# Optimization experiments

Measured on AMD Instinct MI355X. Metric: run time of the kernel, lower is better.

The kernel has to match this reference:

```python
import jax, jax.numpy as jnp
import numpy as np

NUM_EXPERTS = 8
D_MODEL = 768
D_FF = 4 * D_MODEL


def setup_inputs() -> dict:
    key = jax.random.key(0)
    ks = jax.random.split(key, 7)
    s = 0.02
    x = jax.random.normal(ks[0], (2, 1024, D_MODEL), dtype=jnp.float32)
    router_w = jax.random.normal(ks[1], (D_MODEL, NUM_EXPERTS), dtype=jnp.float32) * s
    router_b = jnp.zeros((NUM_EXPERTS,), dtype=jnp.float32)
    w1 = jax.random.normal(ks[2], (NUM_EXPERTS, D_MODEL, D_FF), dtype=jnp.float32) * s
    b1 = jnp.zeros((NUM_EXPERTS, D_FF), dtype=jnp.float32)
    w2 = jax.random.normal(ks[3], (NUM_EXPERTS, D_FF, D_MODEL), dtype=jnp.float32) * s
    b2 = jnp.zeros((NUM_EXPERTS, D_MODEL), dtype=jnp.float32)
    return {"x": x, "router_w": router_w, "router_b": router_b,
            "w1": w1, "b1": b1, "w2": w2, "b2": b2}


def reference(x, router_w, router_b, w1, b1, w2, b2):
    B, S, D = x.shape
    x_flat = x.reshape(-1, D)                      # [T, D]
    logits = x_flat @ router_w + router_b          # [T, E]
    probs = jax.nn.softmax(logits, axis=-1)
    expert_idx = jnp.argmax(probs, axis=-1)        # [T] int, top-1 routing
    onehot = jax.nn.one_hot(expert_idx, NUM_EXPERTS, dtype=x.dtype)  # [T, E]

    # Per-expert FFN; combine via top-1 one-hot (output is NOT scaled by prob,
    # matching the original). Dropout is eval-mode identity.
    out = jnp.zeros_like(x_flat)
    for e in range(NUM_EXPERTS):
        h = jax.nn.relu(x_flat @ w1[e] + b1[e])    # [T, D_FF]
        y = h @ w2[e] + b2[e]                      # [T, D]
        out = out + onehot[:, e:e + 1] * y
    outputs = out.reshape(B, S, D)

    # Load-balance loss: MSE between empirical expert usage and uniform.
    usage = jnp.bincount(expert_idx, length=NUM_EXPERTS).astype(jnp.float32)
    usage = usage / usage.sum()
    uniform = jnp.full((NUM_EXPERTS,), 1.0 / NUM_EXPERTS, dtype=jnp.float32)
    load_balance_loss = jnp.mean((usage - uniform) ** 2)
    return outputs, load_balance_loss
```

## Files before the change

### kernel.cpp

```cpp
#include <hip/hip_runtime.h>
#include <hip/hip_bf16.h>

#define NTOK 2048
#define DMODEL 768
#define DFF 3072
#define NEXP 8
#define MAXT 24

typedef short bf16x8 __attribute__((ext_vector_type(8)));
typedef float f32x4 __attribute__((ext_vector_type(4)));

typedef __attribute__((address_space(1))) const char GCHAR;
typedef __attribute__((address_space(3))) char LCHAR;
#define GL16(g, l) __builtin_amdgcn_global_load_lds((GCHAR*)(g), (LCHAR*)(l), 16, 0, 0)

template <int K, int N>
__device__ void transpose_tile(const float* __restrict__ W, __hip_bfloat16* __restrict__ WT,
                               int e, int k0, int n0, float* T) {
  const int t = threadIdx.x;
  {
    const int kr = t >> 4;
    const int nc = (t & 15) * 4;
    const float* src = W + ((size_t)e * K + k0) * N + n0;
#pragma unroll
    for (int i = 0; i < 4; i++) {
      float4 v = *(const float4*)(src + (size_t)(kr + i * 16) * N + nc);
      T[(kr + i * 16) * 65 + nc + 0] = v.x;
      T[(kr + i * 16) * 65 + nc + 1] = v.y;
      T[(kr + i * 16) * 65 + nc + 2] = v.z;
      T[(kr + i * 16) * 65 + nc + 3] = v.w;
    }
  }
  __syncthreads();
  {
    const int n = t >> 2;
    const int kq = (t & 3) * 16;
    __align__(16) __hip_bfloat16 u[16];
#pragma unroll
    for (int j = 0; j < 16; j++) u[j] = __float2bfloat16(T[(kq + j) * 65 + n]);
    __hip_bfloat16* dst = WT + ((size_t)e * N + n0 + n) * K + k0 + kq;
    *(int4*)dst = *(const int4*)&u[0];
    *(int4*)(dst + 8) = *(const int4*)&u[8];
  }
}

__global__ __launch_bounds__(256) void k_router_t1(
    const float* __restrict__ x, const float* __restrict__ rw,
    const float* __restrict__ rb, __hip_bfloat16* __restrict__ xbf,
    int* __restrict__ eidx, int* __restrict__ cnt,
    const float* __restrict__ w1, __hip_bfloat16* __restrict__ wT1) {
  __shared__ float T[64 * 65];
  if (blockIdx.x >= 512) {
    int tb = blockIdx.x - 512;
    int n_i = tb % (DFF / 64);
    int k_i = (tb / (DFF / 64)) % (DMODEL / 64);
    int e = tb / ((DFF / 64) * (DMODEL / 64));
    transpose_tile<DMODEL, DFF>(w1, wT1, e, k_i * 64, n_i * 64, T);
    return;
  }
  int tok = (blockIdx.x * blockDim.x + threadIdx.x) >> 6;
  int lane = threadIdx.x & 63;
  if (tok >= NTOK) return;
  const float* xr = x + (size_t)tok * DMODEL;
  double acc[NEXP];
#pragma unroll
  for (int e = 0; e < NEXP; e++) acc[e] = 0.0;
  for (int d0 = 0; d0 < DMODEL; d0 += 64) {
    float v = xr[d0 + lane];
    xbf[(size_t)tok * DMODEL + d0 + lane] = __float2bfloat16(v);
    const float* wrow = rw + (size_t)(d0 + lane) * NEXP;
#pragma unroll
    for (int e = 0; e < NEXP; e++) acc[e] += (double)v * (double)wrow[e];
  }
#pragma unroll
  for (int e = 0; e < NEXP; e++) {
    double a = acc[e];
#pragma unroll
    for (int s = 32; s > 0; s >>= 1) a += __shfl_xor(a, s);
    acc[e] = a;
  }
  if (lane == 0) {
    int best = 0;
    double bv = acc[0] + (double)rb[0];
#pragma unroll
    for (int e = 1; e < NEXP; e++) {
      double v = acc[e] + (double)rb[e];
      if (v > bv) { bv = v; best = e; }
    }
    eidx[tok] = best;
    atomicAdd(&cnt[best], 1);
  }
}

__global__ void k_scan(const int* __restrict__ cnt, int* __restrict__ off,
                       int* __restrict__ cur, float* __restrict__ loss,
                       int* __restrict__ tiles, int* __restrict__ ntile) {
  if (threadIdx.x == 0) {
    int s = 0;
    float l = 0.f;
    int nt = 0;
    for (int e = 0; e < NEXP; e++) {
      off[e] = s;
      cur[e] = s;
      for (int m = 0; m < cnt[e]; m += 128) tiles[nt++] = (e << 20) | m;
      s += cnt[e];
      float u = (float)cnt[e] / (float)NTOK - 1.0f / (float)NEXP;
      l += u * u;
    }
    *ntile = nt;
    *loss = l / (float)NEXP;
  }
}

__global__ __launch_bounds__(256) void k_build(const int* __restrict__ eidx,
                                               int* __restrict__ cur,
                                               int* __restrict__ list) {
  int t = blockIdx.x * blockDim.x + threadIdx.x;
  if (t < NTOK) {
    int e = eidx[t];
    int p = atomicAdd(&cur[e], 1);
    list[p] = t;
  }
}

template <int K_TOT, int KCHUNK, int N, int NSPLIT, bool RELU_BF16, bool GATHER_A,
          bool ATOMIC_C, int TK, int TN>
__global__ __launch_bounds__(256) void k_gemm5(
    const __hip_bfloat16* __restrict__ A, const __hip_bfloat16* __restrict__ BT,
    const float* __restrict__ bias, void* __restrict__ Cout,
    const int* __restrict__ cnt, const int* __restrict__ off,
    const int* __restrict__ list, const int* __restrict__ tiles,
    const int* __restrict__ ntile, const float* __restrict__ Tsrc,
    __hip_bfloat16* __restrict__ Tdst) {
  constexpr int NX = N / 128;
  constexpr int W = NX * MAXT * NSPLIT;
  __shared__ __align__(16) char smem[49152];

  if constexpr (TK > 0) {
    if (blockIdx.x >= W) {
      int tb = blockIdx.x - W;
      int n_i = tb % (TN / 64);
      int k_i = (tb / (TN / 64)) % (TK / 64);
      int e = tb / ((TN / 64) * (TK / 64));
      transpose_tile<TK, TN>(Tsrc, Tdst, e, k_i * 64, n_i * 64, (float*)smem);
      return;
    }
  }

  int b = blockIdx.x;
  constexpr int q = W / 8, r = W % 8;
  const int xcd = b & 7, ii = b >> 3;
  const int widx = (xcd < r ? xcd * (q + 1) : r * (q + 1) + (xcd - r) * q) + ii;
  const int split = widx % NSPLIT;
  const int rest = widx / NSPLIT;
  const int ti = rest % MAXT;
  const int nx = rest / MAXT;
  if (ti >= *ntile) return;
  const int tv = tiles[ti];
  const int e = tv >> 20;
  const int m0 = tv & 0xFFFFF;
  const int ce = cnt[e];
  const int oe = off[e];
  const int n0 = nx * 128;
  const int kbase = split * KCHUNK;

  const int tid = threadIdx.x;
  const int lane = tid & 63;
  const int w = tid >> 6;
  const int wr = (w >> 1) * 64;
  const int wc = (w & 1) * 64;
  const int fr = lane & 15;
  const int hi = lane >> 4;

  const int srow = tid >> 2;
  const int cch = (tid & 3) ^ ((tid >> 3) & 3);

  const __hip_bfloat16* ga[2];
#pragma unroll
  for (int j = 0; j < 2; j++) {
    int mr = m0 + j * 64 + srow;
    int src;
    if (GATHER_A) {
      src = list[oe + (mr < ce ? mr : 0)];
    } else {
      int p2 = oe + mr;
      src = p2 < NTOK ? p2 : NTOK - 1;
    }
    ga[j] = A + (size_t)src * K_TOT + kbase + cch * 8;
  }
  const __hip_bfloat16* gb[2];
#pragma unroll
  for (int j = 0; j < 2; j++) {
    int nr = n0 + j * 64 + srow;
    gb[j] = BT + ((size_t)e * N + nr) * K_TOT + kbase + cch * 8;
  }

  char* lA = smem + tid * 16;

  f32x4 acc[4][4] = {};
  constexpr int NT = KCHUNK / 32;

#define STAGE(buf, kc)                                \
  do {                                                \
    GL16(ga[0] + (kc), lA + (buf)*16384 + 0);         \
    GL16(ga[1] + (kc), lA + (buf)*16384 + 4096);      \
    GL16(gb[0] + (kc), lA + (buf)*16384 + 8192);      \
    GL16(gb[1] + (kc), lA + (buf)*16384 + 12288);     \
  } while (0)

  STAGE(0, 0);
  STAGE(1, 32);
  int cur = 0, sb = 2;
  const int xr = (fr >> 1) & 3;
#pragma unroll 1
  for (int t = 0; t < NT; ++t) {
    if (t + 2 < NT) {
      STAGE(sb, (t + 2) * 32);
      asm volatile("s_waitcnt vmcnt(8)" ::: "memory");
    } else if (t + 1 < NT) {
      asm volatile("s_waitcnt vmcnt(4)" ::: "memory");
    } else {
      asm volatile("s_waitcnt vmcnt(0)" ::: "memory");
    }
    __builtin_amdgcn_s_barrier();
    {
      const char* bA = smem + cur * 16384;
      const char* bB = bA + 8192;
      bf16x8 fa[4], fb[4];
#pragma unroll
      for (int mf = 0; mf < 4; mf++) {
        const int row = wr + mf * 16 + fr;
        fa[mf] = *(const bf16x8*)(bA + row * 64 + ((hi ^ xr) * 16));
      }
#pragma unroll
      for (int nf = 0; nf < 4; nf++) {
        const int row = wc + nf * 16 + fr;
        fb[nf] = *(const bf16x8*)(bB + row * 64 + ((hi ^ xr) * 16));
      }
#pragma unroll
      for (int mf = 0; mf < 4; mf++)
#pragma unroll
        for (int nf = 0; nf < 4; nf++)
          acc[mf][nf] = __builtin_amdgcn_mfma_f32_16x16x32_bf16(fa[mf], fb[nf],
                                                                acc[mf][nf], 0, 0, 0);
    }
    __builtin_amdgcn_s_barrier();
    cur = (cur == 2) ? 0 : cur + 1;
    sb = (sb == 2) ? 0 : sb + 1;
  }
#undef STAGE

#pragma unroll
  for (int mf = 0; mf < 4; mf++) {
#pragma unroll
    for (int jj = 0; jj < 4; jj++) {
      const int mloc = m0 + wr + mf * 16 + hi * 4 + jj;
      if (mloc >= ce) continue;
      if (RELU_BF16) {
        __hip_bfloat16* C = (__hip_bfloat16*)Cout;
        size_t row = (size_t)(oe + mloc) * N;
        const float* bi = bias + (size_t)e * N;
#pragma unroll
        for (int nf = 0; nf < 4; nf++) {
          int nn = n0 + wc + nf * 16 + fr;
          float v = acc[mf][nf][jj] + bi[nn];
          C[row + nn] = __float2bfloat16(v > 0.f ? v : 0.f);
        }
      } else {
        float* C = (float*)Cout;
        int tok = list[oe + mloc];
        size_t row = (size_t)tok * N;
        const float* bi = bias + (size_t)e * N;
#pragma unroll
        for (int nf = 0; nf < 4; nf++) {
          int nn = n0 + wc + nf * 16 + fr;
          float v = acc[mf][nf][jj] + (split == 0 ? bi[nn] : 0.f);
          if (ATOMIC_C)
            atomicAdd(&C[row + nn], v);
          else
            C[row + nn] = v;
        }
      }
    }
  }
}

template <int K, int N, bool RELU_BF16, bool GATHER_A, bool SCATTER_C>
__global__ __launch_bounds__(256) void k_gemm(
    const __hip_bfloat16* __restrict__ A, const float* __restrict__ Bw,
    const float* __restrict__ bias, void* __restrict__ Cout,
    const int* __restrict__ cnt, const int* __restrict__ off,
    const int* __restrict__ list) {
  const int e = blockIdx.z;
  const int ce = cnt[e];
  const int m0 = blockIdx.y * 128;
  if (m0 >= ce) return;
  const int oe = off[e];
  const int n0 = blockIdx.x * 128;

  __shared__ __hip_bfloat16 Asm[128][32];
  __shared__ __hip_bfloat16 Bsm[128][32];

  const int tid = threadIdx.x;
  const int ra = tid >> 1;
  const int ha = (tid & 1) * 16;
  size_t arow;
  {
    int mr = m0 + ra;
    int src;
    if (GATHER_A) {
      src = (mr < ce) ? list[oe + mr] : list[oe];
    } else {
      int p = oe + mr;
      src = (p < NTOK) ? p : (NTOK - 1);
    }
    arow = (size_t)src * K;
  }
  const int rbk = tid >> 3;
  const int nb = (tid & 7) * 16;
  const float* bsrc0 = Bw + ((size_t)e * K + rbk) * N + n0 + nb;

  const int w = tid >> 6;
  const int lane = tid & 63;
  const int wr = (w >> 1) * 64;
  const int wc = (w & 1) * 64;
  const int fr = lane & 15;
  const int fk = (lane >> 4) * 8;

  f32x4 acc[4][4] = {};

  for (int k0 = 0; k0 < K; k0 += 32) {
    __syncthreads();
    {
      const __hip_bfloat16* s = A + arow + k0 + ha;
      int4 v0 = *(const int4*)(s);
      int4 v1 = *(const int4*)(s + 8);
      *(int4*)(&Asm[ra][ha]) = v0;
      *(int4*)(&Asm[ra][ha + 8]) = v1;
    }
    {
      const float* s = bsrc0 + (size_t)k0 * N;
      float4 f0 = *(const float4*)(s);
      float4 f1 = *(const float4*)(s + 4);
      float4 f2 = *(const float4*)(s + 8);
      float4 f3 = *(const float4*)(s + 12);
      __hip_bfloat16* dst = &Bsm[nb][0] + rbk;
      dst[0 * 32] = __float2bfloat16(f0.x);
      dst[1 * 32] = __float2bfloat16(f0.y);
      dst[2 * 32] = __float2bfloat16(f0.z);
      dst[3 * 32] = __float2bfloat16(f0.w);
      dst[4 * 32] = __float2bfloat16(f1.x);
      dst[5 * 32] = __float2bfloat16(f1.y);
      dst[6 * 32] = __float2bfloat16(f1.z);
      dst[7 * 32] = __float2bfloat16(f1.w);
      dst[8 * 32] = __float2bfloat16(f2.x);
      dst[9 * 32] = __float2bfloat16(f2.y);
      dst[10 * 32] = __float2bfloat16(f2.z);
      dst[11 * 32] = __float2bfloat16(f2.w);
      dst[12 * 32] = __float2bfloat16(f3.x);
      dst[13 * 32] = __float2bfloat16(f3.y);
      dst[14 * 32] = __float2bfloat16(f3.z);
      dst[15 * 32] = __float2bfloat16(f3.w);
    }
    __syncthreads();

    bf16x8 fa[4], fb[4];
#pragma unroll
    for (int mf = 0; mf < 4; mf++) fa[mf] = *(const bf16x8*)(&Asm[wr + mf * 16 + fr][fk]);
#pragma unroll
    for (int nf = 0; nf < 4; nf++) fb[nf] = *(const bf16x8*)(&Bsm[wc + nf * 16 + fr][fk]);
#pragma unroll
    for (int mf = 0; mf < 4; mf++)
#pragma unroll
      for (int nf = 0; nf < 4; nf++)
        acc[mf][nf] = __builtin_amdgcn_mfma_f32_16x16x32_bf16(fa[mf], fb[nf], acc[mf][nf], 0, 0, 0);
  }

#pragma unroll
  for (int mf = 0; mf < 4; mf++) {
#pragma unroll
    for (int j = 0; j < 4; j++) {
      const int mloc = m0 + wr + mf * 16 + (lane >> 4) * 4 + j;
      if (mloc >= ce) continue;
      if (RELU_BF16) {
        __hip_bfloat16* C = (__hip_bfloat16*)Cout;
        size_t row = (size_t)(oe + mloc) * N;
        const float* bi = bias + (size_t)e * N;
#pragma unroll
        for (int nf = 0; nf < 4; nf++) {
          int nn = n0 + wc + nf * 16 + fr;
          float v = acc[mf][nf][j] + bi[nn];
          C[row + nn] = __float2bfloat16(v > 0.f ? v : 0.f);
        }
      } else {
        float* C = (float*)Cout;
        int tok = SCATTER_C ? list[oe + mloc] : (oe + mloc);
        size_t row = (size_t)tok * N;
        const float* bi = bias + (size_t)e * N;
#pragma unroll
        for (int nf = 0; nf < 4; nf++) {
          int nn = n0 + wc + nf * 16 + fr;
          C[row + nn] = acc[mf][nf][j] + bi[nn];
        }
      }
    }
  }
}

extern "C" void kernel_launch(void* const* d_in, const int* in_sizes, int n_in,
                              void* d_out, int out_size, void* d_ws, size_t ws_size,
                              hipStream_t stream) {
  const float* x = (const float*)d_in[0];
  const float* rw = (const float*)d_in[1];
  const float* rb = (const float*)d_in[2];
  const float* w1 = (const float*)d_in[3];
  const float* b1 = (const float*)d_in[4];
  const float* w2 = (const float*)d_in[5];
  const float* b2 = (const float*)d_in[6];
  float* out = (float*)d_out;

  char* ws = (char*)d_ws;
  int* cnt = (int*)(ws + 0);
  int* off = (int*)(ws + 32);
  int* cur = (int*)(ws + 64);
  int* ntile = (int*)(ws + 96);
  int* tiles = (int*)(ws + 128);
  int* eidx = (int*)(ws + 512);
  int* list = (int*)(ws + 8704);
  __hip_bfloat16* xbf = (__hip_bfloat16*)(ws + 65536);
  __hip_bfloat16* h = (__hip_bfloat16*)(ws + 4194304);
  __hip_bfloat16* wT1 = (__hip_bfloat16*)(ws + 20971520);
  __hip_bfloat16* wT2 = (__hip_bfloat16*)(ws + 58720256);

  float* loss = out + (size_t)2 * 1024 * 768;
  const size_t REQ = 58720256ull + 37748736ull;

  (void)hipMemsetAsync(cnt, 0, 96, stream);
  (void)hipMemsetAsync(d_out, 0, (size_t)out_size * sizeof(float), stream);

  if (ws_size >= REQ) {
    const int TBLK = (DMODEL / 64) * (DFF / 64) * NEXP;
    k_router_t1<<<512 + TBLK, 256, 0, stream>>>(x, rw, rb, xbf, eidx, cnt, w1, wT1);
    k_scan<<<1, 64, 0, stream>>>(cnt, off, cur, loss, tiles, ntile);
    k_build<<<8, 256, 0, stream>>>(eidx, cur, list);
    k_gemm5<DMODEL, DMODEL, DFF, 1, true, true, false, DFF, DMODEL>
        <<<(DFF / 128) * MAXT + TBLK, 256, 0, stream>>>(
            xbf, wT1, b1, h, cnt, off, list, tiles, ntile, w2, wT2);
    k_gemm5<DFF, DFF / 4, DMODEL, 4, false, false, true, 0, 64>
        <<<(DMODEL / 128) * MAXT * 4, 256, 0, stream>>>(
            h, wT2, b2, out, cnt, off, list, tiles, ntile, nullptr, nullptr);
  } else {
    k_router_t1<<<512, 256, 0, stream>>>(x, rw, rb, xbf, eidx, cnt, w1, wT1);
    k_scan<<<1, 64, 0, stream>>>(cnt, off, cur, loss, tiles, ntile);
    k_build<<<8, 256, 0, stream>>>(eidx, cur, list);
    k_gemm<DMODEL, DFF, true, true, false>
        <<<dim3(DFF / 128, 16, NEXP), 256, 0, stream>>>(xbf, w1, b1, h, cnt, off, list);
    k_gemm<DFF, DMODEL, false, false, true>
        <<<dim3(DMODEL / 128, 16, NEXP), 256, 0, stream>>>(h, w2, b2, out, cnt, off, list);
  }
}
```

Before: 152.4 us.

## Fuse fp32 weight conversion into GEMM loads and replace atomics with partial-sum reduce

Drops the separate transpose-to-bf16 passes over w1 and w2. The GEMM now loads fp32 weights directly into registers, converts them to bf16 and writes them swizzled into LDS, using a register-prefetched pipeline four steps deep. The second GEMM writes per-split partial sums to a workspace instead of doing atomicAdd into the output, and a new reduce kernel sums the four splits and adds the bias, which also removes the output memset. The intent is to avoid writing and re-reading bf16 weight copies every call, at the cost of reading fp32 weights and extra partial-buffer traffic and register pressure.

```diff
diff --git a/kernel.cpp b/kernel.cpp
--- a/kernel.cpp
+++ b/kernel.cpp
@@ -14,50 +14,15 @@
 typedef __attribute__((address_space(3))) char LCHAR;
 #define GL16(g, l) __builtin_amdgcn_global_load_lds((GCHAR*)(g), (LCHAR*)(l), 16, 0, 0)
 
-template <int K, int N>
-__device__ void transpose_tile(const float* __restrict__ W, __hip_bfloat16* __restrict__ WT,
-                               int e, int k0, int n0, float* T) {
-  const int t = threadIdx.x;
-  {
-    const int kr = t >> 4;
-    const int nc = (t & 15) * 4;
-    const float* src = W + ((size_t)e * K + k0) * N + n0;
-#pragma unroll
-    for (int i = 0; i < 4; i++) {
-      float4 v = *(const float4*)(src + (size_t)(kr + i * 16) * N + nc);
-      T[(kr + i * 16) * 65 + nc + 0] = v.x;
-      T[(kr + i * 16) * 65 + nc + 1] = v.y;
-      T[(kr + i * 16) * 65 + nc + 2] = v.z;
-      T[(kr + i * 16) * 65 + nc + 3] = v.w;
-    }
-  }
-  __syncthreads();
-  {
-    const int n = t >> 2;
-    const int kq = (t & 3) * 16;
-    __align__(16) __hip_bfloat16 u[16];
-#pragma unroll
-    for (int j = 0; j < 16; j++) u[j] = __float2bfloat16(T[(kq + j) * 65 + n]);
-    __hip_bfloat16* dst = WT + ((size_t)e * N + n0 + n) * K + k0 + kq;
-    *(int4*)dst = *(const int4*)&u[0];
-    *(int4*)(dst + 8) = *(const int4*)&u[8];
-  }
-}
-
-__global__ __launch_bounds__(256) void k_router_t1(
+__device__ __forceinline__ unsigned int bfu(float v) {
+  __hip_bfloat16 b = __float2bfloat16(v);
+  return (unsigned int)*(unsigned short*)&b;
+}
+
+__global__ __launch_bounds__(256) void k_router(
     const float* __restrict__ x, const float* __restrict__ rw,
     const float* __restrict__ rb, __hip_bfloat16* __restrict__ xbf,
-    int* __restrict__ eidx, int* __restrict__ cnt,
-    const float* __restrict__ w1, __hip_bfloat16* __restrict__ wT1) {
-  __shared__ float T[64 * 65];
-  if (blockIdx.x >= 512) {
-    int tb = blockIdx.x - 512;
-    int n_i = tb % (DFF / 64);
-    int k_i = (tb / (DFF / 64)) % (DMODEL / 64);
-    int e = tb / ((DFF / 64) * (DMODEL / 64));
-    transpose_tile<DMODEL, DFF>(w1, wT1, e, k_i * 64, n_i * 64, T);
-    return;
-  }
+    int* __restrict__ eidx, int* __restrict__ cnt) {
   int tok = (blockIdx.x * blockDim.x + threadIdx.x) >> 6;
   int lane = threadIdx.x & 63;
   if (tok >= NTOK) return;
@@ -124,28 +89,17 @@
 }
 
 template <int K_TOT, int KCHUNK, int N, int NSPLIT, bool RELU_BF16, bool GATHER_A,
-          bool ATOMIC_C, int TK, int TN>
-__global__ __launch_bounds__(256) void k_gemm5(
-    const __hip_bfloat16* __restrict__ A, const __hip_bfloat16* __restrict__ BT,
+          bool PART_C>
+__global__ __launch_bounds__(256, 3) void k_gemm7(
+    const __hip_bfloat16* __restrict__ A, const float* __restrict__ Bw,
     const float* __restrict__ bias, void* __restrict__ Cout,
     const int* __restrict__ cnt, const int* __restrict__ off,
     const int* __restrict__ list, const int* __restrict__ tiles,
-    const int* __restrict__ ntile, const float* __restrict__ Tsrc,
-    __hip_bfloat16* __restrict__ Tdst) {
+    const int* __restrict__ ntile) {
   constexpr int NX = N / 128;
   constexpr int W = NX * MAXT * NSPLIT;
+  constexpr int NT = KCHUNK / 32;
   __shared__ __align__(16) char smem[49152];
-
-  if constexpr (TK > 0) {
-    if (blockIdx.x >= W) {
-      int tb = blockIdx.x - W;
-      int n_i = tb % (TN / 64);
-      int k_i = (tb / (TN / 64)) % (TK / 64);
-      int e = tb / ((TN / 64) * (TK / 64));
-      transpose_tile<TK, TN>(Tsrc, Tdst, e, k_i * 64, n_i * 64, (float*)smem);
-      return;
-    }
-  }
 
   int b = blockIdx.x;
   constexpr int q = W / 8, r = W % 8;
@@ -171,10 +125,10 @@
   const int wc = (w & 1) * 64;
   const int fr = lane & 15;
   const int hi = lane >> 4;
+  const int xr = (fr >> 1) & 3;
 
   const int srow = tid >> 2;
   const int cch = (tid & 3) ^ ((tid >> 3) & 3);
-
   const __hip_bfloat16* ga[2];
 #pragma unroll
   for (int j = 0; j < 2; j++) {
@@ -188,67 +142,105 @@
     }
     ga[j] = A + (size_t)src * K_TOT + kbase + cch * 8;
   }
-  const __hip_bfloat16* gb[2];
-#pragma unroll
-  for (int j = 0; j < 2; j++) {
-    int nr = n0 + j * 64 + srow;
-    gb[j] = BT + ((size_t)e * N + nr) * K_TOT + kbase + cch * 8;
-  }
-
-  char* lA = smem + tid * 16;
-
+
+  const int bn = tid >> 1;
+  const int bkg = tid & 1;
+  const float* gB = Bw + ((size_t)e * K_TOT + kbase + bkg * 16) * N + n0 + bn;
+  const int xrn = (bn >> 1) & 3;
+  char* bwp0 = smem + 24576 + bn * 64 + (((bkg * 2 + 0) ^ xrn) * 16);
+  char* bwp1 = smem + 24576 + bn * 64 + (((bkg * 2 + 1) ^ xrn) * 16);
+
+  float f0[16], f1[16];
   f32x4 acc[4][4] = {};
-  constexpr int NT = KCHUNK / 32;
-
-#define STAGE(buf, kc)                                \
-  do {                                                \
-    GL16(ga[0] + (kc), lA + (buf)*16384 + 0);         \
-    GL16(ga[1] + (kc), lA + (buf)*16384 + 4096);      \
-    GL16(gb[0] + (kc), lA + (buf)*16384 + 8192);      \
-    GL16(gb[1] + (kc), lA + (buf)*16384 + 12288);     \
+
+#define STAGEA(buf, kc)                                       \
+  do {                                                        \
+    GL16(ga[0] + (kc), smem + (buf)*8192 + tid * 16);         \
+    GL16(ga[1] + (kc), smem + (buf)*8192 + 4096 + tid * 16);  \
   } while (0)
 
-  STAGE(0, 0);
-  STAGE(1, 32);
-  int cur = 0, sb = 2;
-  const int xr = (fr >> 1) & 3;
-#pragma unroll 1
+#define BLOADM(kstep, F)                                                   \
+  do {                                                                     \
+    const float* s_ = gB + (size_t)(kstep)*32 * N;                         \
+    _Pragma("unroll") for (int i_ = 0; i_ < 16; i_++) F[i_] =              \
+        s_[(size_t)i_ * N];                                                \
+  } while (0)
+
+#define BWRITEM(buf, F)                                                    \
+  do {                                                                     \
+    unsigned int u_[8];                                                    \
+    _Pragma("unroll") for (int i_ = 0; i_ < 8; i_++) u_[i_] =              \
+        bfu(F[2 * i_]) | (bfu(F[2 * i_ + 1]) << 16);                       \
+    *(uint4*)(bwp0 + (buf)*8192) = make_uint4(u_[0], u_[1], u_[2], u_[3]); \
+    *(uint4*)(bwp1 + (buf)*8192) = make_uint4(u_[4], u_[5], u_[6], u_[7]); \
+  } while (0)
+
+#define COMPUTE(buf)                                                          \
+  do {                                                                        \
+    const char* bA = smem + (buf)*8192;                                       \
+    const char* bB = smem + 24576 + (buf)*8192;                               \
+    bf16x8 fa[4], fb[4];                                                      \
+    _Pragma("unroll") for (int mf = 0; mf < 4; mf++) {                        \
+      const int row = wr + mf * 16 + fr;                                      \
+      fa[mf] = *(const bf16x8*)(bA + row * 64 + ((hi ^ xr) * 16));            \
+    }                                                                         \
+    _Pragma("unroll") for (int nf = 0; nf < 4; nf++) {                        \
+      const int row = wc + nf * 16 + fr;                                      \
+      fb[nf] = *(const bf16x8*)(bB + row * 64 + ((hi ^ xr) * 16));            \
+    }                                                                         \
+    _Pragma("unroll") for (int mf = 0; mf < 4; mf++)                          \
+        _Pragma("unroll") for (int nf = 0; nf < 4; nf++) acc[mf][nf] =        \
+            __builtin_amdgcn_mfma_f32_16x16x32_bf16(fa[mf], fb[nf],           \
+                                                    acc[mf][nf], 0, 0, 0);    \
+  } while (0)
+
+  BLOADM(0, f0);
+  BLOADM(1, f1);
+  STAGEA(0, 0);
+  STAGEA(1, 32);
+  asm volatile("s_waitcnt vmcnt(0)" ::: "memory");
+  BWRITEM(0, f0);
+  BLOADM(2, f0);
+  asm volatile("" ::: "memory");
+  BWRITEM(1, f1);
+  BLOADM(3, f1);
+
+#pragma unroll 2
   for (int t = 0; t < NT; ++t) {
+    if (t == 0)
+      asm volatile("s_waitcnt vmcnt(16)" ::: "memory");
+    else if (t <= NT - 4)
+      asm volatile("s_waitcnt vmcnt(18)" ::: "memory");
+    else if (t < NT - 1)
+      asm volatile("s_waitcnt vmcnt(2)" ::: "memory");
+    else
+      asm volatile("s_waitcnt vmcnt(0)" ::: "memory");
+    asm volatile("s_waitcnt lgkmcnt(0)" ::: "memory");
+    __builtin_amdgcn_s_barrier();
+    asm volatile("" ::: "memory");
+    const int curb = t % 3;
+    const int nxb = (t + 2) % 3;
     if (t + 2 < NT) {
-      STAGE(sb, (t + 2) * 32);
-      asm volatile("s_waitcnt vmcnt(8)" ::: "memory");
-    } else if (t + 1 < NT) {
-      asm volatile("s_waitcnt vmcnt(4)" ::: "memory");
-    } else {
-      asm volatile("s_waitcnt vmcnt(0)" ::: "memory");
-    }
-    __builtin_amdgcn_s_barrier();
-    {
-      const char* bA = smem + cur * 16384;
-      const char* bB = bA + 8192;
-      bf16x8 fa[4], fb[4];
-#pragma unroll
-      for (int mf = 0; mf < 4; mf++) {
-        const int row = wr + mf * 16 + fr;
-        fa[mf] = *(const bf16x8*)(bA + row * 64 + ((hi ^ xr) * 16));
+      if (t & 1) {
+        BWRITEM(nxb, f1);
+      } else {
+        BWRITEM(nxb, f0);
       }
-#pragma unroll
-      for (int nf = 0; nf < 4; nf++) {
-        const int row = wc + nf * 16 + fr;
-        fb[nf] = *(const bf16x8*)(bB + row * 64 + ((hi ^ xr) * 16));
+      STAGEA(nxb, (t + 2) * 32);
+    }
+    if (t + 4 < NT) {
+      if (t & 1) {
+        BLOADM(t + 4, f1);
+      } else {
+        BLOADM(t + 4, f0);
       }
-#pragma unroll
-      for (int mf = 0; mf < 4; mf++)
-#pragma unroll
-        for (int nf = 0; nf < 4; nf++)
-          acc[mf][nf] = __builtin_amdgcn_mfma_f32_16x16x32_bf16(fa[mf], fb[nf],
-                                                                acc[mf][nf], 0, 0, 0);
-    }
-    __builtin_amdgcn_s_barrier();
-    cur = (cur == 2) ? 0 : cur + 1;
-    sb = (sb == 2) ? 0 : sb + 1;
-  }
-#undef STAGE
+    }
+    COMPUTE(curb);
+  }
+#undef STAGEA
+#undef BLOADM
+#undef BWRITEM
+#undef COMPUTE
 
 #pragma unroll
   for (int mf = 0; mf < 4; mf++) {
@@ -269,20 +261,37 @@
       } else {
         float* C = (float*)Cout;
         int tok = list[oe + mloc];
-        size_t row = (size_t)tok * N;
-        const float* bi = bias + (size_t)e * N;
+        size_t row = ((size_t)split * NTOK + tok) * N;
 #pragma unroll
         for (int nf = 0; nf < 4; nf++) {
           int nn = n0 + wc + nf * 16 + fr;
-          float v = acc[mf][nf][jj] + (split == 0 ? bi[nn] : 0.f);
-          if (ATOMIC_C)
-            atomicAdd(&C[row + nn], v);
-          else
-            C[row + nn] = v;
+          C[row + nn] = acc[mf][nf][jj];
         }
       }
     }
   }
+}
+
+__global__ __launch_bounds__(256) void k_reduce(const float* __restrict__ p,
+                                                const float* __restrict__ b2,
+                                                const int* __restrict__ eidx,
+                                                float* __restrict__ out) {
+  const int idx = blockIdx.x * 256 + threadIdx.x;
+  const int base = idx * 4;
+  const int tok = base / DMODEL;
+  const int n = base - tok * DMODEL;
+  const int e = eidx[tok];
+  float4 a = *(const float4*)(p + (size_t)0 * NTOK * DMODEL + base);
+  float4 c = *(const float4*)(p + (size_t)1 * NTOK * DMODEL + base);
+  float4 d = *(const float4*)(p + (size_t)2 * NTOK * DMODEL + base);
+  float4 g = *(const float4*)(p + (size_t)3 * NTOK * DMODEL + base);
+  float4 bb = *(const float4*)(b2 + (size_t)e * DMODEL + n);
+  float4 o;
+  o.x = a.x + c.x + d.x + g.x + bb.x;
+  o.y = a.y + c.y + d.y + g.y + bb.y;
+  o.z = a.z + c.z + d.z + g.z + bb.z;
+  o.w = a.w + c.w + d.w + g.w + bb.w;
+  *(float4*)(out + base) = o;
 }
 
 template <int K, int N, bool RELU_BF16, bool GATHER_A, bool SCATTER_C>
@@ -340,27 +349,27 @@
     }
     {
       const float* s = bsrc0 + (size_t)k0 * N;
-      float4 f0 = *(const float4*)(s);
-      float4 f1 = *(const float4*)(s + 4);
-      float4 f2 = *(const float4*)(s + 8);
-      float4 f3 = *(const float4*)(s + 12);
+      float4 q0 = *(const float4*)(s);
+      float4 q1 = *(const float4*)(s + 4);
+      float4 q2 = *(const float4*)(s + 8);
+      float4 q3 = *(const float4*)(s + 12);
       __hip_bfloat16* dst = &Bsm[nb][0] + rbk;
-      dst[0 * 32] = __float2bfloat16(f0.x);
-      dst[1 * 32] = __float2bfloat16(f0.y);
-      dst[2 * 32] = __float2bfloat16(f0.z);
-      dst[3 * 32] = __float2bfloat16(f0.w);
-      dst[4 * 32] = __float2bfloat16(f1.x);
-      dst[5 * 32] = __float2bfloat16(f1.y);
-      dst[6 * 32] = __float2bfloat16(f1.z);
-      dst[7 * 32] = __float2bfloat16(f1.w);
-      dst[8 * 32] = __float2bfloat16(f2.x);
-      dst[9 * 32] = __float2bfloat16(f2.y);
-      dst[10 * 32] = __float2bfloat16(f2.z);
-      dst[11 * 32] = __float2bfloat16(f2.w);
-      dst[12 * 32] = __float2bfloat16(f3.x);
-      dst[13 * 32] = __float2bfloat16(f3.y);
-      dst[14 * 32] = __float2bfloat16(f3.z);
-      dst[15 * 32] = __float2bfloat16(f3.w);
+      dst[0 * 32] = __float2bfloat16(q0.x);
+      dst[1 * 32] = __float2bfloat16(q0.y);
+      dst[2 * 32] = __float2bfloat16(q0.z);
+      dst[3 * 32] = __float2bfloat16(q0.w);
+      dst[4 * 32] = __float2bfloat16(q1.x);
+      dst[5 * 32] = __float2bfloat16(q1.y);
+      dst[6 * 32] = __float2bfloat16(q1.z);
+      dst[7 * 32] = __float2bfloat16(q1.w);
+      dst[8 * 32] = __float2bfloat16(q2.x);
+      dst[9 * 32] = __float2bfloat16(q2.y);
+      dst[10 * 32] = __float2bfloat16(q2.z);
+      dst[11 * 32] = __float2bfloat16(q2.w);
+      dst[12 * 32] = __float2bfloat16(q3.x);
+      dst[13 * 32] = __float2bfloat16(q3.y);
+      dst[14 * 32] = __float2bfloat16(q3.z);
+      dst[15 * 32] = __float2bfloat16(q3.w);
     }
     __syncthreads();
 
@@ -429,30 +438,28 @@
   int* list = (int*)(ws + 8704);
   __hip_bfloat16* xbf = (__hip_bfloat16*)(ws + 65536);
   __hip_bfloat16* h = (__hip_bfloat16*)(ws + 4194304);
-  __hip_bfloat16* wT1 = (__hip_bfloat16*)(ws + 20971520);
-  __hip_bfloat16* wT2 = (__hip_bfloat16*)(ws + 58720256);
+  float* part = (float*)(ws + 16777216);
 
   float* loss = out + (size_t)2 * 1024 * 768;
-  const size_t REQ = 58720256ull + 37748736ull;
+  const size_t REQ = 16777216ull + 25165824ull;
 
   (void)hipMemsetAsync(cnt, 0, 96, stream);
-  (void)hipMemsetAsync(d_out, 0, (size_t)out_size * sizeof(float), stream);
+  if (ws_size < REQ)
+    (void)hipMemsetAsync(d_out, 0, (size_t)out_size * sizeof(float), stream);
+
+  k_router<<<512, 256, 0, stream>>>(x, rw, rb, xbf, eidx, cnt);
+  k_scan<<<1, 64, 0, stream>>>(cnt, off, cur, loss, tiles, ntile);
+  k_build<<<8, 256, 0, stream>>>(eidx, cur, list);
 
   if (ws_size >= REQ) {
-    const int TBLK = (DMODEL / 64) * (DFF / 64) * NEXP;
-    k_router_t1<<<512 + TBLK, 256, 0, stream>>>(x, rw, rb, xbf, eidx, cnt, w1, wT1);
-    k_scan<<<1, 64, 0, stream>>>(cnt, off, cur, loss, tiles, ntile);
-    k_build<<<8, 256, 0, stream>>>(eidx, cur, list);
-    k_gemm5<DMODEL, DMODEL, DFF, 1, true, true, false, DFF, DMODEL>
-        <<<(DFF / 128) * MAXT + TBLK, 256, 0, stream>>>(
-            xbf, wT1, b1, h, cnt, off, list, tiles, ntile, w2, wT2);
-    k_gemm5<DFF, DFF / 4, DMODEL, 4, false, false, true, 0, 64>
-        <<<(DMODEL / 128) * MAXT * 4, 256, 0, stream>>>(
-            h, wT2, b2, out, cnt, off, list, tiles, ntile, nullptr, nullptr);
+    k_gemm7<DMODEL, DMODEL, DFF, 1, true, true, false>
+        <<<(DFF / 128) * MAXT, 256, 0, stream>>>(xbf, w1, b1, h, cnt, off, list,
+                                                 tiles, ntile);
+    k_gemm7<DFF, DFF / 4, DMODEL, 4, false, false, true>
+        <<<(DMODEL / 128) * MAXT * 4, 256, 0, stream>>>(h, w2, nullptr, part, cnt,
+                                                        off, list, tiles, ntile);
+    k_reduce<<<(NTOK * DMODEL) / 1024, 256, 0, stream>>>(part, b2, eidx, out);
   } else {
-    k_router_t1<<<512, 256, 0, stream>>>(x, rw, rb, xbf, eidx, cnt, w1, wT1);
-    k_scan<<<1, 64, 0, stream>>>(cnt, off, cur, loss, tiles, ntile);
-    k_build<<<8, 256, 0, stream>>>(eidx, cur, list);
     k_gemm<DMODEL, DFF, true, true, false>
         <<<dim3(DFF / 128, 16, NEXP), 256, 0, stream>>>(xbf, w1, b1, h, cnt, off, list);
     k_gemm<DFF, DMODEL, false, false, true>
```

New measurement: 162.6 us. 1.07x slower.
